# Performance work log

Hardware: AMD Instinct MI355X
Metric: run time of the kernel (lower is better)

## Reference

```python
import jax, jax.numpy as jnp
import numpy as np

B, T = 1024, 128
T_IN, A_IN, V_IN = 300, 74, 35
D = 128            # dim_capsule
H = D // 2
ROUTING = 3
LABEL = 1


def _glorot(key, shape):
    fan_out, fan_in = shape[-2], shape[-1]
    s = jnp.sqrt(2.0 / (fan_in + fan_out)).astype(jnp.float32)
    return jax.random.normal(key, shape, jnp.float32) * s


def setup_inputs() -> dict:
    k = iter(jax.random.split(jax.random.key(0), 40))
    inp = {}
    inp["text"] = jax.random.normal(next(k), (B, T, T_IN), jnp.float32)
    inp["audio"] = jax.random.normal(next(k), (B, T, A_IN), jnp.float32)
    inp["video"] = jax.random.normal(next(k), (B, T, V_IN), jnp.float32)
    # bidirectional encoder LSTMs (hidden = D//2 per direction); biases b = b_ih + b_hh
    for p, din in (("t", T_IN), ("a", A_IN), ("v", V_IN)):
        for d in ("f", "b"):
            inp[p + "_Wih_" + d] = _glorot(next(k), (4 * H, din))
            inp[p + "_Whh_" + d] = _glorot(next(k), (4 * H, H))
            inp[p + "_b_" + d] = jnp.zeros((4 * H,), jnp.float32)
    # 4 capsule projection matrices per modality, stacked [4, D, D]
    inp["Wt"] = _glorot(next(k), (4, D, D))
    inp["Wa"] = _glorot(next(k), (4, D, D))
    inp["Wv"] = _glorot(next(k), (4, D, D))
    # routing LSTMs (ta, tv, av, tav) stacked on leading axis
    inp["r_Wih"] = _glorot(next(k), (4, 4 * D, D))
    inp["r_Whh"] = _glorot(next(k), (4, 4 * D, D))
    inp["r_b"] = jnp.zeros((4, 4 * D), jnp.float32)
    # decision bidirectional LSTM (hidden = D per direction)
    for d in ("f", "b"):
        inp["d_Wih_" + d] = _glorot(next(k), (4 * D, D))
        inp["d_Whh_" + d] = _glorot(next(k), (4 * D, D))
        inp["d_b_" + d] = jnp.zeros((4 * D,), jnp.float32)
    inp["fc1_W"] = _glorot(next(k), (H, D))
    inp["fc1_b"] = jnp.zeros((H,), jnp.float32)
    inp["fc2_W"] = _glorot(next(k), (LABEL, H))
    inp["fc2_b"] = jnp.zeros((LABEL,), jnp.float32)
    inp["batch_size"] = B
    return inp


def _lstm_final(x, Wih, Whh, b):
    # x: [B, T, I] -> final hidden state [B, Hh]; torch gate order i, f, g, o
    Hh = Whh.shape[-1]
    z = jnp.zeros((x.shape[0], Hh), x.dtype)

    def step(carry, xt):
        h, c = carry
        g = xt @ Wih.T + h @ Whh.T + b
        i, f, gg, o = jnp.split(g, 4, axis=-1)
        c = jax.nn.sigmoid(f) * c + jax.nn.sigmoid(i) * jnp.tanh(gg)
        h = jax.nn.sigmoid(o) * jnp.tanh(c)
        return (h, c), None

    (h, _), _ = jax.lax.scan(step, (z, z), jnp.swapaxes(x, 0, 1))
    return h


def _forward(text, audio, video,
             t_Wih_f, t_Whh_f, t_b_f, t_Wih_b, t_Whh_b, t_b_b,
             a_Wih_f, a_Whh_f, a_b_f, a_Wih_b, a_Whh_b, a_b_b,
             v_Wih_f, v_Whh_f, v_b_f, v_Wih_b, v_Whh_b, v_b_b,
             Wt, Wa, Wv, r_Wih, r_Whh, r_b,
             d_Wih_f, d_Whh_f, d_b_f, d_Wih_b, d_Whh_b, d_b_b,
             fc1_W, fc1_b, fc2_W, fc2_b):
    Bsz = text.shape[0]

    def ctx(x, Wf, Uf, bf, Wb, Ub, bb):
        # biLSTM final hidden, fwd||bwd concat -> [B, 1, D]
        hf = _lstm_final(x, Wf, Uf, bf)
        hb = _lstm_final(x[:, ::-1], Wb, Ub, bb)
        return jnp.concatenate([hf, hb], -1)[:, None, :]

    tc = ctx(text, t_Wih_f, t_Whh_f, t_b_f, t_Wih_b, t_Whh_b, t_b_b)
    ac = ctx(audio, a_Wih_f, a_Whh_f, a_b_f, a_Wih_b, a_Whh_b, a_b_b)
    vc = ctx(video, v_Wih_f, v_Whh_f, v_b_f, v_Wih_b, v_Whh_b, v_b_b)

    tusc = jnp.einsum('bod,kde->kboe', tc, Wt)   # [4, B, 1, D]
    ausc = jnp.einsum('bod,kde->kboe', ac, Wa)
    vusc = jnp.einsum('bod,kde->kboe', vc, Wv)

    pre = [jnp.concatenate([tusc[0], ausc[0]], 1),                # ta  [B,2,D]
           jnp.concatenate([tusc[1], vusc[0]], 1),                # tv  [B,2,D]
           jnp.concatenate([ausc[1], vusc[1]], 1),                # av  [B,2,D]
           jnp.concatenate([tusc[2], ausc[2], vusc[2]], 1)]       # tav [B,3,D]

    rc = [jnp.ones((Bsz, n, D), text.dtype) for n in (2, 2, 2, 3, 7)]
    dc = None
    for r in range(ROUTING + 1):
        rc = [jax.nn.softmax(c, axis=1) for c in rc]
        # per-pair routing LSTMs, final hidden [B,1,D]
        bc = [_lstm_final(rc[i] * pre[i], r_Wih[i], r_Whh[i], r_b[i])[:, None, :]
              for i in range(4)]
        deci = jnp.concatenate([tusc[3], ausc[3], vusc[3]] + bc, 1)  # [B,7,D]
        xd = rc[4] * deci
        # decision biLSTM: sum of both directions' final hidden -> [B,1,D]
        dc = (_lstm_final(xd, d_Wih_f, d_Whh_f, d_b_f)
              + _lstm_final(xd[:, ::-1], d_Wih_b, d_Whh_b, d_b_b))[:, None, :]
        if r < ROUTING:
            # agreement update: bmm gives [B,n,1], broadcasts over last dim (== repeat)
            rc = [rc[i] + jnp.matmul(pre[i], jnp.swapaxes(bc[i], 1, 2)) for i in range(4)] \
                 + [rc[4] + jnp.matmul(deci, jnp.swapaxes(dc, 1, 2))]

    dc = dc[:, 0, :]
    o1 = jnp.tanh(dc @ fc1_W.T + fc1_b)
    return o1 @ fc2_W.T + fc2_b   # mosi: no output tanh


def reference(text, audio, video,
              t_Wih_f, t_Whh_f, t_b_f, t_Wih_b, t_Whh_b, t_b_b,
              a_Wih_f, a_Whh_f, a_b_f, a_Wih_b, a_Whh_b, a_b_b,
              v_Wih_f, v_Whh_f, v_b_f, v_Wih_b, v_Whh_b, v_b_b,
              Wt, Wa, Wv, r_Wih, r_Whh, r_b,
              d_Wih_f, d_Whh_f, d_b_f, d_Wih_b, d_Whh_b, d_b_b,
              fc1_W, fc1_b, fc2_W, fc2_b, batch_size):
    return _forward(text, audio, video,
                    t_Wih_f, t_Whh_f, t_b_f, t_Wih_b, t_Whh_b, t_b_b,
                    a_Wih_f, a_Whh_f, a_b_f, a_Wih_b, a_Whh_b, a_b_b,
                    v_Wih_f, v_Whh_f, v_b_f, v_Wih_b, v_Whh_b, v_b_b,
                    Wt, Wa, Wv, r_Wih, r_Whh, r_b,
                    d_Wih_f, d_Whh_f, d_b_f, d_Wih_b, d_Whh_b, d_b_b,
                    fc1_W, fc1_b, fc2_W, fc2_b)
```

## Files before the change

### kernel.cpp

```cpp
#include <hip/hip_runtime.h>

typedef __bf16 bf16;
typedef _Float16 f16;
typedef f16 f16x8 __attribute__((ext_vector_type(8)));
typedef float f32x4 __attribute__((ext_vector_type(4)));

__device__ __forceinline__ f32x4 mfma16h(f16x8 a, f16x8 b, f32x4 c) {
  return __builtin_amdgcn_mfma_f32_16x16x32_f16(a, b, c, 0, 0, 0);
}
__device__ __forceinline__ float sigm(float x) { return 1.0f / (1.0f + __expf(-x)); }
__device__ __forceinline__ float tanh_f(float x) {
  float e = __expf(-2.0f * fabsf(x));
  return copysignf((1.0f - e) / (1.0f + e), x);
}
__device__ __forceinline__ float ldin(const void* p, long i, int f32m) {
  if (f32m) return ((const float*)p)[i];
  unsigned u = (unsigned)((const unsigned short*)p)[i] << 16;
  return __uint_as_float(u);
}
__device__ __forceinline__ unsigned short f16u(f16 h) { return __builtin_bit_cast(unsigned short, h); }
__device__ __forceinline__ float bfc(unsigned short s) { return __uint_as_float((unsigned)s << 16); }

__global__ void detect_dtype(const unsigned short* __restrict__ p, int* __restrict__ flag) {
  __shared__ int cnt;
  if (threadIdx.x == 0) cnt = 0;
  __syncthreads();
  int c = 0;
  for (int i = threadIdx.x; i < 4096; i += 256) {
    unsigned e = (p[2 * i] >> 7) & 0xFFu;
    if (e >= 0xC0u) ++c;
  }
  atomicAdd(&cnt, c);
  __syncthreads();
  if (threadIdx.x == 0) *flag = (cnt > 64) ? 1 : 0;
}


struct PadArgs { const void* src[6]; };
__global__ void conv_pad(PadArgs a, f16* __restrict__ wo, const int* __restrict__ flag) {
  const int dinT[6] = {300, 300, 74, 74, 35, 35};
  const int kpT[6] = {320, 320, 96, 96, 64, 64};
  const int offT[6] = {0, 81920, 163840, 188416, 212992, 229376};
  int id = blockIdx.y;
  int din = dinT[id], kp = kpT[id];
  const void* s = a.src[id];
  f16* o = wo + offT[id];
  int f32m = *flag;
  int total = 256 * kp;
  for (int i = blockIdx.x * blockDim.x + threadIdx.x; i < total; i += gridDim.x * blockDim.x) {
    int n = i / kp, k = i - n * kp;
    float v = (k < din) ? ldin(s, n * din + k, f32m) : 0.0f;
    o[i] = (f16)v;
  }
}

struct HiloArgs { const void* src[12]; int n[12]; int off[12]; };
__global__ void conv_h16(HiloArgs a, f16* __restrict__ wo, const int* __restrict__ flag) {
  int j = blockIdx.y;
  int n = a.n[j];
  const void* s = a.src[j];
  f16* o = wo + a.off[j];
  int f32m = *flag;
  for (int i = blockIdx.x * blockDim.x + threadIdx.x; i < n; i += gridDim.x * blockDim.x)
    o[i] = (f16)ldin(s, i, f32m);
}

struct F32Args { const void* src[16]; int n[16]; int off[16]; };
__global__ void conv_f32(F32Args a, float* __restrict__ dst, const int* __restrict__ flag) {
  int j = blockIdx.y;
  int n = a.n[j];
  const void* s = a.src[j];
  float* d = dst + a.off[j];
  int f32m = *flag;
  for (int i = blockIdx.x * blockDim.x + threadIdx.x; i < n; i += gridDim.x * blockDim.x)
    d[i] = ldin(s, i, f32m);
}

__global__ void init_rc(float* __restrict__ rcs) {
  int i = blockIdx.x * 256 + threadIdx.x;
  if (i < 16384) rcs[i] = 1.0f;
}

struct TriArgs {
  const void* x[3];
  const f16* wAll;
  const float* fmisc;
  float* ctx;
  const int* flag;
};

template <int DIN, int KP, int CHUNK, int F32M>
__device__ void tri_body(const void* __restrict__ xsrc,
                         const f16* __restrict__ wp, const f16* __restrict__ whh,
                         const float* __restrict__ bias, float* __restrict__ ctx,
                         int m, int d, int b0, char* sm) {
  constexpr int XP = KP + 8;
  constexpr int NKS = KP / 32;
  constexpr int NCH = DIN / CHUNK;
  constexpr int ITER = (NCH + 15) / 16;

  f16 (*Xhi)[XP] = (f16 (*)[XP])sm;
  f16 (*Xlo)[XP] = (f16 (*)[XP])(sm + 32 * XP * 2);
  f16 (*hbuf)[16][72] = (f16 (*)[16][72])(sm + 64 * XP * 2);
  float* gbuf = (float*)(sm + 64 * XP * 2 + 4608);

  const int tid = threadIdx.x;
  const int lane = tid & 63, n16 = lane & 15, q = lane >> 4, w8 = tid >> 6;
  const int srow = tid & 31, sct = tid >> 5;
  const int hc = tid & 63, rr = tid >> 6;

  f16x8 wihr[2][NKS];
  f16x8 whr[2][2];
#pragma unroll
  for (int t = 0; t < 2; ++t) {
    int cc = (w8 + t * 8) * 16 + n16;
#pragma unroll
    for (int ks = 0; ks < NKS; ++ks)
      wihr[t][ks] = *(const f16x8*)(wp + cc * KP + ks * 32 + q * 8);
#pragma unroll
    for (int ks = 0; ks < 2; ++ks)
      whr[t][ks] = *(const f16x8*)(whh + cc * 64 + ks * 32 + q * 8);
  }
  float bgm[4];
#pragma unroll
  for (int g = 0; g < 4; ++g) bgm[g] = bias[g * 64 + hc];

  {
    unsigned* z = (unsigned*)sm;
    int nz = (64 * XP * 2 + 4608) >> 2;
    for (int i = tid; i < nz; i += 512) z[i] = 0u;
  }

  uint4 pf[ITER];
  auto stage_load = [&](int tg) {
#pragma unroll
    for (int i = 0; i < ITER; ++i) {
      int c = sct + i * 16;
      if (c < NCH) {
        int tl = srow >> 4, bb = srow & 15;
        int t = tg * 2 + tl; if (d) t = 127 - t;
        long base = ((long)(b0 + bb) * 128 + t) * DIN + c * CHUNK;
        if (F32M) {
          const float* p = (const float*)xsrc + base;
          if constexpr (CHUNK == 4) pf[i] = *(const uint4*)p;
          else if constexpr (CHUNK == 2) { uint2 v = *(const uint2*)p; pf[i].x = v.x; pf[i].y = v.y; }
          else pf[i].x = *(const unsigned*)p;
        } else {
          const unsigned short* p = (const unsigned short*)xsrc + base;
          if constexpr (CHUNK == 4) { uint2 v = *(const uint2*)p; pf[i].x = v.x; pf[i].y = v.y; }
          else if constexpr (CHUNK == 2) pf[i].x = *(const unsigned*)p;
          else pf[i].x = *p;
        }
      }
    }
  };
  auto stage_store = [&]() {
#pragma unroll
    for (int i = 0; i < ITER; ++i) {
      int c = sct + i * 16;
      if (c < NCH) {
        float v[4];
        if (F32M) {
          v[0] = __uint_as_float(pf[i].x); v[1] = __uint_as_float(pf[i].y);
// ... 84 lines not shown
      float c = sigm(gf) * c2[e] + sigm(gi) * tanh_f(gg);
      c2[e] = c;
      float h = sigm(go) * tanh_f(c);
      hbuf[1][row][hc] = (f16)h;
    }
    __syncthreads();

    {
      f16x8 h0 = *(const f16x8*)(&hbuf[1][n16][q * 8]);
      f16x8 h1 = *(const f16x8*)(&hbuf[1][n16][32 + q * 8]);
      a10 = mfma16h(h0, whr[0][0], a10); a10 = mfma16h(h1, whr[0][1], a10);
      a11 = mfma16h(h0, whr[1][0], a11); a11 = mfma16h(h1, whr[1][1], a11);
    }
#pragma unroll
    for (int e = 0; e < 4; ++e) {
      gbuf[(q * 4 + e) * 260 + w8 * 16 + n16] = a10[e];
      gbuf[(q * 4 + e) * 260 + 128 + w8 * 16 + n16] = a11[e];
    }
    __syncthreads();

    const bool lastStep = (tg == 63);
#pragma unroll
    for (int e = 0; e < 2; ++e) {
      int row = rr + e * 8;
      float gi = gbuf[row * 260 + hc] + bgm[0];
      float gf = gbuf[row * 260 + 64 + hc] + bgm[1];
      float gg = gbuf[row * 260 + 128 + hc] + bgm[2];
      float go = gbuf[row * 260 + 192 + hc] + bgm[3];
      float c = sigm(gf) * c2[e] + sigm(gi) * tanh_f(gg);
      c2[e] = c;
      float h = sigm(go) * tanh_f(c);
      hbuf[0][row][hc] = (f16)h;
      if (lastStep) ctx[(m * 1024 + b0 + row) * 128 + d * 64 + hc] = h;
    }
  }
}

__global__ __launch_bounds__(512, 2) void tri_lstm(TriArgs A) {
  __shared__ __align__(16) char sm[64 * 328 * 2 + 4608 + 16640];
  int bid = blockIdx.x;
  int md = bid >> 6, xb = bid & 63;
  int m = md >> 1, d = md & 1, b0 = xb * 16;
  const int wpOffT[6] = {0, 81920, 163840, 188416, 212992, 229376};
  const f16* wp = A.wAll + wpOffT[md];
  const f16* whh = A.wAll + 245760 + md * 16384;
  const float* bias = A.fmisc + md * 256;
  int f32m = *A.flag;
  if (f32m) {
    if (m == 0)      tri_body<300, 320, 4, 1>(A.x[0], wp, whh, bias, A.ctx, m, d, b0, sm);
    else if (m == 1) tri_body<74, 96, 2, 1>(A.x[1], wp, whh, bias, A.ctx, m, d, b0, sm);
    else             tri_body<35, 64, 1, 1>(A.x[2], wp, whh, bias, A.ctx, m, d, b0, sm);
  } else {
    if (m == 0)      tri_body<300, 320, 4, 0>(A.x[0], wp, whh, bias, A.ctx, m, d, b0, sm);
    else if (m == 1) tri_body<74, 96, 2, 0>(A.x[1], wp, whh, bias, A.ctx, m, d, b0, sm);
    else             tri_body<35, 64, 1, 0>(A.x[2], wp, whh, bias, A.ctx, m, d, b0, sm);
  }
}

__global__ __launch_bounds__(128) void usc_kern(const float* __restrict__ ctx,
                                                const float* __restrict__ fmisc,
                                                float* __restrict__ usc) {
  __shared__ float cr[4][128];
  int b0 = blockIdx.x * 4;
  int mk = blockIdx.y, mod = mk >> 2;
  int e = threadIdx.x;
  const float* W = fmisc + 4608 + mk * 16384;
  for (int i = e; i < 512; i += 128) {
    int r = i >> 7, dd = i & 127;
    cr[r][dd] = ctx[(mod * 1024 + b0 + r) * 128 + dd];
  }
  __syncthreads();
  float a0 = 0.f, a1 = 0.f, a2 = 0.f, a3 = 0.f;
  for (int dd = 0; dd < 128; ++dd) {
    float wv = W[dd * 128 + e];
    a0 += cr[0][dd] * wv; a1 += cr[1][dd] * wv;
    a2 += cr[2][dd] * wv; a3 += cr[3][dd] * wv;
  }
  usc[(mk * 1024 + b0 + 0) * 128 + e] = a0;
  usc[(mk * 1024 + b0 + 1) * 128 + e] = a1;
  usc[(mk * 1024 + b0 + 2) * 128 + e] = a2;
  usc[(mk * 1024 + b0 + 3) * 128 + e] = a3;
}

#define LSTM_STEP_DECL \
  const int tid = threadIdx.x; \
  const int lane = tid & 63, n16 = lane & 15, q = lane >> 4, w = tid >> 6; \
  const int u = w * 16 + n16; \
  const int u2 = tid & 127, rgg = tid >> 7;

__device__ __forceinline__ void lstm_step_mfma(
    f32x4* acc, const f16 (*xh)[16][136], const f16 (*xl)[16][136],
    const f16 (*hh)[16][136], int p,
    const f16* __restrict__ Wih, const f16x8 (*whf)[4],
    int n16, int q, int u) {
#pragma unroll
  for (int ks = 0; ks < 4; ++ks) {
    f16x8 axh = *(const f16x8*)(&xh[p][n16][ks * 32 + q * 8]);
    f16x8 axl = *(const f16x8*)(&xl[p][n16][ks * 32 + q * 8]);
    f16x8 ahh = *(const f16x8*)(&hh[p][n16][ks * 32 + q * 8]);
#pragma unroll
    for (int g = 0; g < 4; ++g) {
      f16x8 bh = *(const f16x8*)(Wih + (g * 128 + u) * 128 + ks * 32 + q * 8);
      acc[g] = mfma16h(axh, bh, acc[g]);
      acc[g] = mfma16h(axl, bh, acc[g]);
      acc[g] = mfma16h(ahh, whf[g][ks], acc[g]);
    }
  }
}

__global__ __launch_bounds__(512) void rchain(const float* __restrict__ usc,
                                              const float* __restrict__ rcs,
                                              const f16* __restrict__ wAll,
                                              const float* __restrict__ fmisc,
                                              float* __restrict__ bcg) {
  __shared__ __align__(16) f16 xh[2][16][136], xl[2][16][136], hh[2][16][136];
  __shared__ float rcl[16][3];
  LSTM_STEP_DECL
  const int chain = blockIdx.y;
  const int b0 = blockIdx.x * 16;
  const int WihOff[4] = {344064, 409600, 475136, 540672};
  const int WhhOff[4] = {606208, 671744, 737280, 802816};
  const int bOff[4] = {1536, 2048, 2560, 3072};
  const int ns = (chain == 3) ? 3 : 2;

  if (tid < 16) {
    int row = tid;
    int goff = (chain == 3) ? 6 : chain * 2;
    float v[3], mx = -1e30f;
    for (int j = 0; j < ns; ++j) { v[j] = rcs[(b0 + row) * 16 + goff + j]; mx = fmaxf(mx, v[j]); }
    float s = 0.f;
    for (int j = 0; j < ns; ++j) { v[j] = __expf(v[j] - mx); s += v[j]; }
    float inv = 1.0f / s;
    for (int j = 0; j < ns; ++j) rcl[row][j] = v[j] * inv;
  }
  for (int i = tid; i < 2 * 16 * 136; i += 512) (&hh[0][0][0])[i] = (f16)0.0f;

  const f16* Whh = wAll + WhhOff[chain];
  f16x8 whf[4][4];
#pragma unroll
  for (int g = 0; g < 4; ++g)
#pragma unroll
    for (int ks = 0; ks < 4; ++ks)
      whf[g][ks] = *(const f16x8*)(Whh + (g * 128 + u) * 128 + ks * 32 + q * 8);
  const f16* Wih = wAll + WihOff[chain];
  const float* bias = fmisc + bOff[chain];
  float bg[4];
#pragma unroll
  for (int g = 0; g < 4; ++g) bg[g] = bias[g * 128 + u];

  const int preMk0[4] = {0, 1, 5, 2};
  const int preMk1[4] = {4, 8, 9, 6};
  float creg[4] = {0.f, 0.f, 0.f, 0.f};
  __syncthreads();

  for (int s = 0; s < ns; ++s) {
    int p = s & 1;
    int mk = (s == 0) ? preMk0[chain] : (s == 1 ? preMk1[chain] : 10);
#pragma unroll
    for (int rr = 0; rr < 4; ++rr) {
      int row = rgg * 4 + rr;
      float pv = usc[(mk * 1024 + b0 + row) * 128 + u2];
      float xv = rcl[row][s] * pv;
      f16 xhv = (f16)xv;
      xh[p][row][u2] = xhv;
      xl[p][row][u2] = (f16)(xv - (float)xhv);
    }
    __syncthreads();
    f32x4 acc[4];
    const f32x4 zf = {0.f, 0.f, 0.f, 0.f};
#pragma unroll
    for (int g = 0; g < 4; ++g) acc[g] = zf;
    lstm_step_mfma(acc, xh, xl, hh, p, Wih, whf, n16, q, u);
#pragma unroll
    for (int e = 0; e < 4; ++e) {
      int row = q * 4 + e;
      float gi = acc[0][e] + bg[0];
      float gf = acc[1][e] + bg[1];
      float gg = acc[2][e] + bg[2];
      float go = acc[3][e] + bg[3];
      float c = sigm(gf) * creg[e] + sigm(gi) * tanh_f(gg);
      creg[e] = c;
      float h = sigm(go) * tanh_f(c);
      hh[p ^ 1][row][u] = (f16)h;
      if (s == ns - 1) bcg[(chain * 1024 + b0 + row) * 128 + u] = h;
    }
  }
}

__global__ __launch_bounds__(512) void decision(const float* __restrict__ usc,
                                                const float* __restrict__ rcs,
                                                const f16* __restrict__ wAll,
                                                const float* __restrict__ fmisc,
                                                const float* __restrict__ bcg,
                                                float* __restrict__ dcF,
                                                float* __restrict__ dcB) {
  __shared__ __align__(16) f16 xh[2][16][136], xl[2][16][136], hh[2][16][136];
  __shared__ float rcl[16][7];
  LSTM_STEP_DECL
  const int dir = blockIdx.y;
  const int b0 = blockIdx.x * 16;

  if (tid < 16) {
    int row = tid;
    float v[7], mx = -1e30f;
    for (int j = 0; j < 7; ++j) { v[j] = rcs[(b0 + row) * 16 + 9 + j]; mx = fmaxf(mx, v[j]); }
    float s = 0.f;
    for (int j = 0; j < 7; ++j) { v[j] = __expf(v[j] - mx); s += v[j]; }
    float inv = 1.0f / s;
    for (int j = 0; j < 7; ++j) rcl[row][j] = v[j] * inv;
  }
  for (int i = tid; i < 2 * 16 * 136; i += 512) (&hh[0][0][0])[i] = (f16)0.0f;

  const int WihOffD[2] = {868352, 999424};
  const int WhhOffD[2] = {933888, 1064960};
  const int bOffD[2] = {3584, 4096};
  const f16* Whh = wAll + WhhOffD[dir];
  f16x8 whf[4][4];
#pragma unroll
  for (int g = 0; g < 4; ++g)
#pragma unroll
    for (int ks = 0; ks < 4; ++ks)
      whf[g][ks] = *(const f16x8*)(Whh + (g * 128 + u) * 128 + ks * 32 + q * 8);
  const f16* Wih = wAll + WihOffD[dir];
  const float* bias = fmisc + bOffD[dir];
  float bg[4];
#pragma unroll
  for (int g = 0; g < 4; ++g) bg[g] = bias[g * 128 + u];

  const int dmk[3] = {3, 7, 11};
  float creg[4] = {0.f, 0.f, 0.f, 0.f};
  __syncthreads();

  for (int s = 0; s < 7; ++s) {
    int p = s & 1;
    int j = dir ? (6 - s) : s;
#pragma unroll
    for (int rr = 0; rr < 4; ++rr) {
      int row = rgg * 4 + rr;
      float pv = (j < 3) ? usc[(dmk[j] * 1024 + b0 + row) * 128 + u2]
                         : bcg[((j - 3) * 1024 + b0 + row) * 128 + u2];
      float xv = rcl[row][j] * pv;
      f16 xhv = (f16)xv;
      xh[p][row][u2] = xhv;
      xl[p][row][u2] = (f16)(xv - (float)xhv);
    }
    __syncthreads();
    f32x4 acc[4];
    const f32x4 zf = {0.f, 0.f, 0.f, 0.f};
#pragma unroll
    for (int g = 0; g < 4; ++g) acc[g] = zf;
    lstm_step_mfma(acc, xh, xl, hh, p, Wih, whf, n16, q, u);
#pragma unroll
    for (int e = 0; e < 4; ++e) {
      int row = q * 4 + e;
      float gi = acc[0][e] + bg[0];
      float gf = acc[1][e] + bg[1];
      float gg = acc[2][e] + bg[2];
      float go = acc[3][e] + bg[3];
      float c = sigm(gf) * creg[e] + sigm(gi) * tanh_f(gg);
      creg[e] = c;
      float h = sigm(go) * tanh_f(c);
      hh[p ^ 1][row][u] = (f16)h;
      if (s == 6) {
        if (dir == 0) dcF[(b0 + row) * 128 + u] = h;
        else dcB[(b0 + row) * 128 + u] = h;
      }
    }
  }
}

__global__ __launch_bounds__(256) void rupdate(const float* __restrict__ usc,
                                               const float* __restrict__ bcg,
                                               const float* __restrict__ dcF,
                                               const float* __restrict__ dcB,
                                               float* __restrict__ rcs,
                                               float* __restrict__ dcw, int last) {
  __shared__ float dsum[16][128];
  __shared__ float rcl[16][16];
  const int tid = threadIdx.x;
  const int b0 = blockIdx.x * 16;
  for (int i = tid; i < 2048; i += 256) {
    int row = i >> 7, col = i & 127;
    float v = dcF[(b0 + row) * 128 + col] + dcB[(b0 + row) * 128 + col];
    dsum[row][col] = v;
    if (last) dcw[(b0 + row) * 128 + col] = v;
  }
  {
    int row = tid >> 4, cap = tid & 15;
    rcl[row][cap] = rcs[(b0 + row) * 16 + cap];
  }
  __syncthreads();
  if (!last) {
    int row = tid >> 4, cap = tid & 15;
    const int goffT[16] = {0, 0, 2, 2, 4, 4, 6, 6, 6, 9, 9, 9, 9, 9, 9, 9};
    const int gnT[16] = {2, 2, 2, 2, 2, 2, 3, 3, 3, 7, 7, 7, 7, 7, 7, 7};
    int go = goffT[cap], gn = gnT[cap];
    float mx = -1e30f;
    for (int j = 0; j < gn; ++j) mx = fmaxf(mx, rcl[row][go + j]);
    float s = 0.f;
    for (int j = 0; j < gn; ++j) s += __expf(rcl[row][go + j] - mx);
    float sm = __expf(rcl[row][cap] - mx) / s;

    const int preMkTab[9] = {0, 4, 1, 8, 5, 9, 2, 6, 10};
    float a = 0.f;
    if (cap < 9) {
      int i = (cap < 6) ? (cap >> 1) : 3;
      const float* pr = usc + (preMkTab[cap] * 1024 + b0 + row) * 128;
      const float* bcrow = bcg + (i * 1024 + b0 + row) * 128;
      for (int dd = 0; dd < 128; ++dd) a += pr[dd] * bcrow[dd];
    } else {
      int j = cap - 9;
      if (j < 3) {
        const int dmk[3] = {3, 7, 11};
        const float* pr = usc + (dmk[j] * 1024 + b0 + row) * 128;
        for (int dd = 0; dd < 128; ++dd) a += pr[dd] * dsum[row][dd];
      } else {
        const float* bcrow = bcg + ((j - 3) * 1024 + b0 + row) * 128;
        for (int dd = 0; dd < 128; ++dd) a += bcrow[dd] * dsum[row][dd];
      }
    }
    rcs[(b0 + row) * 16 + cap] = sm + a;
  }
}

__global__ __launch_bounds__(64) void head(const float* __restrict__ dc, const float* __restrict__ fcw,
                                           void* __restrict__ out, const int* __restrict__ flag) {
  int b = blockIdx.x, j = threadIdx.x;
  const float* r = dc + b * 128;
  float acc = fcw[209408 + j];
  for (int dd = 0; dd < 128; ++dd) acc += r[dd] * fcw[201216 + j * 128 + dd];
  float o = tanh_f(acc) * fcw[209472 + j];
  for (int off = 32; off; off >>= 1) o += __shfl_down(o, off, 64);
  if (j == 0) {
    float res = o + fcw[209536];
    if (*flag) ((float*)out)[b] = res;
    else ((bf16*)out)[b] = (bf16)res;
  }
}

extern "C" void kernel_launch(void* const* d_in, const int* in_sizes, int n_in,
                              void* d_out, int out_size, void* d_ws, size_t ws_size,
                              hipStream_t stream) {
  float* fw = (float*)d_ws;
  int* flag = (int*)d_ws;
  float* ctx = fw + 4;
  float* usc = ctx + 393216;
  float* dcw = usc + 1572864;
  float* fmisc = dcw + 131072;
  float* rcs = fmisc + 209552;
  float* bcg = rcs + 16384;
  float* dcF = bcg + 524288;
  float* dcB = dcF + 131072;
  f16* wAll = (f16*)(dcB + 131072);

  hipLaunchKernelGGL(detect_dtype, dim3(1), dim3(256), 0, stream,
                     (const unsigned short*)d_in[0], flag);

  PadArgs pa;
  HiloArgs ha;
  for (int m = 0; m < 3; ++m)
    for (int dd = 0; dd < 2; ++dd) {
      int md = m * 6 + dd * 3;
      pa.src[m * 2 + dd] = d_in[3 + md + 0];
      ha.src[m * 2 + dd] = d_in[3 + md + 1];
      ha.n[m * 2 + dd] = 16384;
      ha.off[m * 2 + dd] = 245760 + (m * 2 + dd) * 16384;
    }
  const int hsrc[6] = {24, 25, 27, 28, 30, 31};
  const int hn[6] = {262144, 262144, 65536, 65536, 65536, 65536};
  const int hoff[6] = {344064, 606208, 868352, 933888, 999424, 1064960};
  for (int j = 0; j < 6; ++j) { ha.src[6 + j] = d_in[hsrc[j]]; ha.n[6 + j] = hn[j]; ha.off[6 + j] = hoff[j]; }
  hipLaunchKernelGGL(conv_pad, dim3(64, 6), dim3(256), 0, stream, pa, wAll, (const int*)flag);
  hipLaunchKernelGGL(conv_h16, dim3(128, 12), dim3(256), 0, stream, ha, wAll, (const int*)flag);

  F32Args fa;
  for (int m = 0; m < 3; ++m)
    for (int dd = 0; dd < 2; ++dd) {
      fa.src[m * 2 + dd] = d_in[3 + m * 6 + dd * 3 + 2];
      fa.n[m * 2 + dd] = 256;
      fa.off[m * 2 + dd] = (m * 2 + dd) * 256;
    }
  const int fsrc[10] = {26, 29, 32, 21, 22, 23, 33, 34, 35, 36};
  const int fn[10] = {2048, 512, 512, 65536, 65536, 65536, 8192, 64, 64, 1};
  const int foff[10] = {1536, 3584, 4096, 4608, 70144, 135680, 201216, 209408, 209472, 209536};
  for (int j = 0; j < 10; ++j) { fa.src[6 + j] = d_in[fsrc[j]]; fa.n[6 + j] = fn[j]; fa.off[6 + j] = foff[j]; }
  hipLaunchKernelGGL(conv_f32, dim3(64, 16), dim3(256), 0, stream, fa, fmisc, (const int*)flag);
  hipLaunchKernelGGL(init_rc, dim3(64), dim3(256), 0, stream, rcs);

  TriArgs ta;
  ta.x[0] = d_in[0]; ta.x[1] = d_in[1]; ta.x[2] = d_in[2];
  ta.wAll = wAll; ta.fmisc = fmisc; ta.ctx = ctx; ta.flag = flag;
  hipLaunchKernelGGL(tri_lstm, dim3(384), dim3(512), 0, stream, ta);

  hipLaunchKernelGGL(usc_kern, dim3(256, 12), dim3(128), 0, stream,
                     (const float*)ctx, (const float*)fmisc, usc);

  for (int r = 0; r < 4; ++r) {
    hipLaunchKernelGGL(rchain, dim3(64, 4), dim3(512), 0, stream,
                       (const float*)usc, (const float*)rcs, (const f16*)wAll,
                       (const float*)fmisc, bcg);
    hipLaunchKernelGGL(decision, dim3(64, 2), dim3(512), 0, stream,
                       (const float*)usc, (const float*)rcs, (const f16*)wAll,
                       (const float*)fmisc, (const float*)bcg, dcF, dcB);
    hipLaunchKernelGGL(rupdate, dim3(64), dim3(256), 0, stream,
                       (const float*)usc, (const float*)bcg, (const float*)dcF,
                       (const float*)dcB, rcs, dcw, (r == 3) ? 1 : 0);
  }

  hipLaunchKernelGGL(head, dim3(1024), dim3(64), 0, stream,
                     (const float*)dcw, (const float*)fmisc, d_out, (const int*)flag);
}
```

Measured before the change: 848.2 us.

## Fuse routing iterations into one persistent per-batch-tile kernel

```diff
diff --git a/kernel.cpp b/kernel.cpp
--- a/kernel.cpp
+++ b/kernel.cpp
@@ -74,11 +74,6 @@
   int f32m = *flag;
   for (int i = blockIdx.x * blockDim.x + threadIdx.x; i < n; i += gridDim.x * blockDim.x)
     d[i] = ldin(s, i, f32m);
-}
-
-__global__ void init_rc(float* __restrict__ rcs) {
-  int i = blockIdx.x * 256 + threadIdx.x;
-  if (i < 16384) rcs[i] = 1.0f;
 }
 
 struct TriArgs {
@@ -329,12 +324,6 @@
   usc[(mk * 1024 + b0 + 3) * 128 + e] = a3;
 }
 
-#define LSTM_STEP_DECL \
-  const int tid = threadIdx.x; \
-  const int lane = tid & 63, n16 = lane & 15, q = lane >> 4, w = tid >> 6; \
-  const int u = w * 16 + n16; \
-  const int u2 = tid & 127, rgg = tid >> 7;
-
 __device__ __forceinline__ void lstm_step_mfma(
     f32x4* acc, const f16 (*xh)[16][136], const f16 (*xl)[16][136],
     const f16 (*hh)[16][136], int p,
@@ -355,218 +344,208 @@
   }
 }
 
-__global__ __launch_bounds__(512) void rchain(const float* __restrict__ usc,
-                                              const float* __restrict__ rcs,
-                                              const f16* __restrict__ wAll,
-                                              const float* __restrict__ fmisc,
-                                              float* __restrict__ bcg) {
+__global__ __launch_bounds__(512) void routing(const float* __restrict__ usc,
+                                               const f16* __restrict__ wAll,
+                                               const float* __restrict__ fmisc,
+                                               float* __restrict__ bcg,
+                                               float* __restrict__ dcw) {
   __shared__ __align__(16) f16 xh[2][16][136], xl[2][16][136], hh[2][16][136];
-  __shared__ float rcl[16][3];
-  LSTM_STEP_DECL
-  const int chain = blockIdx.y;
+  __shared__ float rcsS[16][16];
+  __shared__ float rclC[16][7];
+  __shared__ float dcFs[16][128], dcBs[16][128];
+  const int tid = threadIdx.x;
+  const int lane = tid & 63, n16 = lane & 15, q = lane >> 4, w = tid >> 6;
+  const int u = w * 16 + n16;
+  const int u2 = tid & 127, rgg = tid >> 7;
   const int b0 = blockIdx.x * 16;
+
   const int WihOff[4] = {344064, 409600, 475136, 540672};
   const int WhhOff[4] = {606208, 671744, 737280, 802816};
   const int bOff[4] = {1536, 2048, 2560, 3072};
-  const int ns = (chain == 3) ? 3 : 2;
-
-  if (tid < 16) {
-    int row = tid;
-    int goff = (chain == 3) ? 6 : chain * 2;
-    float v[3], mx = -1e30f;
-    for (int j = 0; j < ns; ++j) { v[j] = rcs[(b0 + row) * 16 + goff + j]; mx = fmaxf(mx, v[j]); }
-    float s = 0.f;
-    for (int j = 0; j < ns; ++j) { v[j] = __expf(v[j] - mx); s += v[j]; }
-    float inv = 1.0f / s;
-    for (int j = 0; j < ns; ++j) rcl[row][j] = v[j] * inv;
-  }
-  for (int i = tid; i < 2 * 16 * 136; i += 512) (&hh[0][0][0])[i] = (f16)0.0f;
-
-  const f16* Whh = wAll + WhhOff[chain];
-  f16x8 whf[4][4];
-#pragma unroll
-  for (int g = 0; g < 4; ++g)
-#pragma unroll
-    for (int ks = 0; ks < 4; ++ks)
-      whf[g][ks] = *(const f16x8*)(Whh + (g * 128 + u) * 128 + ks * 32 + q * 8);
-  const f16* Wih = wAll + WihOff[chain];
-  const float* bias = fmisc + bOff[chain];
-  float bg[4];
-#pragma unroll
-  for (int g = 0; g < 4; ++g) bg[g] = bias[g * 128 + u];
-
   const int preMk0[4] = {0, 1, 5, 2};
   const int preMk1[4] = {4, 8, 9, 6};
-  float creg[4] = {0.f, 0.f, 0.f, 0.f};
-  __syncthreads();
-
-  for (int s = 0; s < ns; ++s) {
-    int p = s & 1;
-    int mk = (s == 0) ? preMk0[chain] : (s == 1 ? preMk1[chain] : 10);
-#pragma unroll
-    for (int rr = 0; rr < 4; ++rr) {
-      int row = rgg * 4 + rr;
-      float pv = usc[(mk * 1024 + b0 + row) * 128 + u2];
-      float xv = rcl[row][s] * pv;
-      f16 xhv = (f16)xv;
-      xh[p][row][u2] = xhv;
-      xl[p][row][u2] = (f16)(xv - (float)xhv);
-    }
-    __syncthreads();
-    f32x4 acc[4];
-    const f32x4 zf = {0.f, 0.f, 0.f, 0.f};
-#pragma unroll
-    for (int g = 0; g < 4; ++g) acc[g] = zf;
-    lstm_step_mfma(acc, xh, xl, hh, p, Wih, whf, n16, q, u);
-#pragma unroll
-    for (int e = 0; e < 4; ++e) {
-      int row = q * 4 + e;
-      float gi = acc[0][e] + bg[0];
-      float gf = acc[1][e] + bg[1];
-      float gg = acc[2][e] + bg[2];
-      float go = acc[3][e] + bg[3];
-      float c = sigm(gf) * creg[e] + sigm(gi) * tanh_f(gg);
-      creg[e] = c;
-      float h = sigm(go) * tanh_f(c);
-      hh[p ^ 1][row][u] = (f16)h;
-      if (s == ns - 1) bcg[(chain * 1024 + b0 + row) * 128 + u] = h;
-    }
-  }
-}
-
-__global__ __launch_bounds__(512) void decision(const float* __restrict__ usc,
-                                                const float* __restrict__ rcs,
-                                                const f16* __restrict__ wAll,
-                                                const float* __restrict__ fmisc,
-                                                const float* __restrict__ bcg,
-                                                float* __restrict__ dcF,
-                                                float* __restrict__ dcB) {
-  __shared__ __align__(16) f16 xh[2][16][136], xl[2][16][136], hh[2][16][136];
-  __shared__ float rcl[16][7];
-  LSTM_STEP_DECL
-  const int dir = blockIdx.y;
-  const int b0 = blockIdx.x * 16;
-
-  if (tid < 16) {
-    int row = tid;
-    float v[7], mx = -1e30f;
-    for (int j = 0; j < 7; ++j) { v[j] = rcs[(b0 + row) * 16 + 9 + j]; mx = fmaxf(mx, v[j]); }
-    float s = 0.f;
-    for (int j = 0; j < 7; ++j) { v[j] = __expf(v[j] - mx); s += v[j]; }
-    float inv = 1.0f / s;
-    for (int j = 0; j < 7; ++j) rcl[row][j] = v[j] * inv;
-  }
-  for (int i = tid; i < 2 * 16 * 136; i += 512) (&hh[0][0][0])[i] = (f16)0.0f;
-
+  const int dmk[3] = {3, 7, 11};
   const int WihOffD[2] = {868352, 999424};
   const int WhhOffD[2] = {933888, 1064960};
   const int bOffD[2] = {3584, 4096};
-  const f16* Whh = wAll + WhhOffD[dir];
-  f16x8 whf[4][4];
-#pragma unroll
-  for (int g = 0; g < 4; ++g)
-#pragma unroll
-    for (int ks = 0; ks < 4; ++ks)
-      whf[g][ks] = *(const f16x8*)(Whh + (g * 128 + u) * 128 + ks * 32 + q * 8);
-  const f16* Wih = wAll + WihOffD[dir];
-  const float* bias = fmisc + bOffD[dir];
-  float bg[4];
-#pragma unroll
-  for (int g = 0; g < 4; ++g) bg[g] = bias[g * 128 + u];
-
-  const int dmk[3] = {3, 7, 11};
-  float creg[4] = {0.f, 0.f, 0.f, 0.f};
-  __syncthreads();
-
-  for (int s = 0; s < 7; ++s) {
-    int p = s & 1;
-    int j = dir ? (6 - s) : s;
-#pragma unroll
-    for (int rr = 0; rr < 4; ++rr) {
-      int row = rgg * 4 + rr;
-      float pv = (j < 3) ? usc[(dmk[j] * 1024 + b0 + row) * 128 + u2]
-                         : bcg[((j - 3) * 1024 + b0 + row) * 128 + u2];
-      float xv = rcl[row][j] * pv;
-      f16 xhv = (f16)xv;
-      xh[p][row][u2] = xhv;
-      xl[p][row][u2] = (f16)(xv - (float)xhv);
-    }
-    __syncthreads();
-    f32x4 acc[4];
-    const f32x4 zf = {0.f, 0.f, 0.f, 0.f};
-#pragma unroll
-    for (int g = 0; g < 4; ++g) acc[g] = zf;
-    lstm_step_mfma(acc, xh, xl, hh, p, Wih, whf, n16, q, u);
-#pragma unroll
-    for (int e = 0; e < 4; ++e) {
-      int row = q * 4 + e;
-      float gi = acc[0][e] + bg[0];
-      float gf = acc[1][e] + bg[1];
-      float gg = acc[2][e] + bg[2];
-      float go = acc[3][e] + bg[3];
-      float c = sigm(gf) * creg[e] + sigm(gi) * tanh_f(gg);
-      creg[e] = c;
-      float h = sigm(go) * tanh_f(c);
-      hh[p ^ 1][row][u] = (f16)h;
-      if (s == 6) {
-        if (dir == 0) dcF[(b0 + row) * 128 + u] = h;
-        else dcB[(b0 + row) * 128 + u] = h;
-      }
-    }
-  }
-}
-
-__global__ __launch_bounds__(256) void rupdate(const float* __restrict__ usc,
-                                               const float* __restrict__ bcg,
-                                               const float* __restrict__ dcF,
-                                               const float* __restrict__ dcB,
-                                               float* __restrict__ rcs,
-                                               float* __restrict__ dcw, int last) {
-  __shared__ float dsum[16][128];
-  __shared__ float rcl[16][16];
-  const int tid = threadIdx.x;
-  const int b0 = blockIdx.x * 16;
-  for (int i = tid; i < 2048; i += 256) {
-    int row = i >> 7, col = i & 127;
-    float v = dcF[(b0 + row) * 128 + col] + dcB[(b0 + row) * 128 + col];
-    dsum[row][col] = v;
-    if (last) dcw[(b0 + row) * 128 + col] = v;
-  }
-  {
-    int row = tid >> 4, cap = tid & 15;
-    rcl[row][cap] = rcs[(b0 + row) * 16 + cap];
-  }
-  __syncthreads();
-  if (!last) {
-    int row = tid >> 4, cap = tid & 15;
-    const int goffT[16] = {0, 0, 2, 2, 4, 4, 6, 6, 6, 9, 9, 9, 9, 9, 9, 9};
-    const int gnT[16] = {2, 2, 2, 2, 2, 2, 3, 3, 3, 7, 7, 7, 7, 7, 7, 7};
-    int go = goffT[cap], gn = gnT[cap];
-    float mx = -1e30f;
-    for (int j = 0; j < gn; ++j) mx = fmaxf(mx, rcl[row][go + j]);
-    float s = 0.f;
-    for (int j = 0; j < gn; ++j) s += __expf(rcl[row][go + j] - mx);
-    float sm = __expf(rcl[row][cap] - mx) / s;
-
-    const int preMkTab[9] = {0, 4, 1, 8, 5, 9, 2, 6, 10};
-    float a = 0.f;
-    if (cap < 9) {
-      int i = (cap < 6) ? (cap >> 1) : 3;
-      const float* pr = usc + (preMkTab[cap] * 1024 + b0 + row) * 128;
-      const float* bcrow = bcg + (i * 1024 + b0 + row) * 128;
-      for (int dd = 0; dd < 128; ++dd) a += pr[dd] * bcrow[dd];
+
+  if (tid < 256) rcsS[tid >> 4][tid & 15] = 1.0f;
+
+  for (int r = 0; r < 4; ++r) {
+    for (int chain = 0; chain < 4; ++chain) {
+      const int ns = (chain == 3) ? 3 : 2;
+      __syncthreads();
+      if (tid < 16) {
+        int row = tid;
+        int goff = (chain == 3) ? 6 : chain * 2;
+        float v[3], mx = -1e30f;
+        for (int j = 0; j < ns; ++j) { v[j] = rcsS[row][goff + j]; mx = fmaxf(mx, v[j]); }
+        float s = 0.f;
+        for (int j = 0; j < ns; ++j) { v[j] = __expf(v[j] - mx); s += v[j]; }
+        float inv = 1.0f / s;
+        for (int j = 0; j < ns; ++j) rclC[row][j] = v[j] * inv;
+      }
+      for (int i = tid; i < 2 * 16 * 136; i += 512) (&hh[0][0][0])[i] = (f16)0.0f;
+
+      const f16* Whh = wAll + WhhOff[chain];
+      f16x8 whf[4][4];
+#pragma unroll
+      for (int g = 0; g < 4; ++g)
+#pragma unroll
+        for (int ks = 0; ks < 4; ++ks)
+          whf[g][ks] = *(const f16x8*)(Whh + (g * 128 + u) * 128 + ks * 32 + q * 8);
+      const f16* Wih = wAll + WihOff[chain];
+      const float* bias = fmisc + bOff[chain];
+      float bg[4];
+#pragma unroll
+      for (int g = 0; g < 4; ++g) bg[g] = bias[g * 128 + u];
+
+      float creg[4] = {0.f, 0.f, 0.f, 0.f};
+      __syncthreads();
+
+      for (int s = 0; s < ns; ++s) {
+        int p = s & 1;
+        int mk = (s == 0) ? preMk0[chain] : (s == 1 ? preMk1[chain] : 10);
+#pragma unroll
+        for (int rr = 0; rr < 4; ++rr) {
+          int row = rgg * 4 + rr;
+          float pv = usc[(mk * 1024 + b0 + row) * 128 + u2];
+          float xv = rclC[row][s] * pv;
+          f16 xhv = (f16)xv;
+          xh[p][row][u2] = xhv;
+          xl[p][row][u2] = (f16)(xv - (float)xhv);
+        }
+        __syncthreads();
+        f32x4 acc[4];
+        const f32x4 zf = {0.f, 0.f, 0.f, 0.f};
+#pragma unroll
+        for (int g = 0; g < 4; ++g) acc[g] = zf;
+        lstm_step_mfma(acc, xh, xl, hh, p, Wih, whf, n16, q, u);
+#pragma unroll
+        for (int e = 0; e < 4; ++e) {
+          int row = q * 4 + e;
+          float gi = acc[0][e] + bg[0];
+          float gf = acc[1][e] + bg[1];
+          float gg = acc[2][e] + bg[2];
+          float go = acc[3][e] + bg[3];
+          float c = sigm(gf) * creg[e] + sigm(gi) * tanh_f(gg);
+          creg[e] = c;
+          float h = sigm(go) * tanh_f(c);
+          hh[p ^ 1][row][u] = (f16)h;
+          if (s == ns - 1) bcg[(chain * 1024 + b0 + row) * 128 + u] = h;
+        }
+      }
+      __syncthreads();
+    }
+
+    for (int dir = 0; dir < 2; ++dir) {
+      __syncthreads();
+      if (tid < 16) {
+        int row = tid;
+        float v[7], mx = -1e30f;
+        for (int j = 0; j < 7; ++j) { v[j] = rcsS[row][9 + j]; mx = fmaxf(mx, v[j]); }
+        float s = 0.f;
+        for (int j = 0; j < 7; ++j) { v[j] = __expf(v[j] - mx); s += v[j]; }
+        float inv = 1.0f / s;
+        for (int j = 0; j < 7; ++j) rclC[row][j] = v[j] * inv;
+      }
+      for (int i = tid; i < 2 * 16 * 136; i += 512) (&hh[0][0][0])[i] = (f16)0.0f;
+
+      const f16* Whh = wAll + WhhOffD[dir];
+      f16x8 whf[4][4];
+#pragma unroll
+      for (int g = 0; g < 4; ++g)
+#pragma unroll
+        for (int ks = 0; ks < 4; ++ks)
+          whf[g][ks] = *(const f16x8*)(Whh + (g * 128 + u) * 128 + ks * 32 + q * 8);
+      const f16* Wih = wAll + WihOffD[dir];
+      const float* bias = fmisc + bOffD[dir];
+      float bg[4];
+#pragma unroll
+      for (int g = 0; g < 4; ++g) bg[g] = bias[g * 128 + u];
+
+      float creg[4] = {0.f, 0.f, 0.f, 0.f};
+      __syncthreads();
+
+      for (int s = 0; s < 7; ++s) {
+        int p = s & 1;
+        int j = dir ? (6 - s) : s;
+#pragma unroll
+        for (int rr = 0; rr < 4; ++rr) {
+          int row = rgg * 4 + rr;
+          float pv = (j < 3) ? usc[(dmk[j] * 1024 + b0 + row) * 128 + u2]
+                             : bcg[((j - 3) * 1024 + b0 + row) * 128 + u2];
+          float xv = rclC[row][j] * pv;
+          f16 xhv = (f16)xv;
+          xh[p][row][u2] = xhv;
+          xl[p][row][u2] = (f16)(xv - (float)xhv);
+        }
+        __syncthreads();
+        f32x4 acc[4];
+        const f32x4 zf = {0.f, 0.f, 0.f, 0.f};
+#pragma unroll
+        for (int g = 0; g < 4; ++g) acc[g] = zf;
+        lstm_step_mfma(acc, xh, xl, hh, p, Wih, whf, n16, q, u);
+#pragma unroll
+        for (int e = 0; e < 4; ++e) {
+          int row = q * 4 + e;
+          float gi = acc[0][e] + bg[0];
+          float gf = acc[1][e] + bg[1];
+          float gg = acc[2][e] + bg[2];
+          float go = acc[3][e] + bg[3];
+          float c = sigm(gf) * creg[e] + sigm(gi) * tanh_f(gg);
+          creg[e] = c;
+          float h = sigm(go) * tanh_f(c);
+          hh[p ^ 1][row][u] = (f16)h;
+          if (s == 6) {
+            if (dir == 0) dcFs[row][u] = h;
+            else dcBs[row][u] = h;
+          }
+        }
+      }
+      __syncthreads();
+    }
+
+    if (r == 3) {
+      for (int i = tid; i < 2048; i += 512) {
+        int row = i >> 7, col = i & 127;
+        dcw[(b0 + row) * 128 + col] = dcFs[row][col] + dcBs[row][col];
+      }
     } else {
-      int j = cap - 9;
-      if (j < 3) {
-        const int dmk[3] = {3, 7, 11};
-        const float* pr = usc + (dmk[j] * 1024 + b0 + row) * 128;
-        for (int dd = 0; dd < 128; ++dd) a += pr[dd] * dsum[row][dd];
-      } else {
-        const float* bcrow = bcg + ((j - 3) * 1024 + b0 + row) * 128;
-        for (int dd = 0; dd < 128; ++dd) a += bcrow[dd] * dsum[row][dd];
-      }
-    }
-    rcs[(b0 + row) * 16 + cap] = sm + a;
+      float newv = 0.f;
+      int row = tid >> 4, cap = tid & 15;
+      if (tid < 256) {
+        const int goffT[16] = {0, 0, 2, 2, 4, 4, 6, 6, 6, 9, 9, 9, 9, 9, 9, 9};
+        const int gnT[16] = {2, 2, 2, 2, 2, 2, 3, 3, 3, 7, 7, 7, 7, 7, 7, 7};
+        int go = goffT[cap], gn = gnT[cap];
+        float mx = -1e30f;
+        for (int j = 0; j < gn; ++j) mx = fmaxf(mx, rcsS[row][go + j]);
+        float s = 0.f;
+        for (int j = 0; j < gn; ++j) s += __expf(rcsS[row][go + j] - mx);
+        float sm = __expf(rcsS[row][cap] - mx) / s;
+
+        const int preMkTab[9] = {0, 4, 1, 8, 5, 9, 2, 6, 10};
+        float a = 0.f;
+        if (cap < 9) {
+          int i = (cap < 6) ? (cap >> 1) : 3;
+          const float* pr = usc + (preMkTab[cap] * 1024 + b0 + row) * 128;
+          const float* bcrow = bcg + (i * 1024 + b0 + row) * 128;
+          for (int dd = 0; dd < 128; ++dd) a += pr[dd] * bcrow[dd];
+        } else {
+          int j = cap - 9;
+          if (j < 3) {
+            const float* pr = usc + (dmk[j] * 1024 + b0 + row) * 128;
+            for (int dd = 0; dd < 128; ++dd) a += pr[dd] * (dcFs[row][dd] + dcBs[row][dd]);
+          } else {
+            const float* bcrow = bcg + ((j - 3) * 1024 + b0 + row) * 128;
+            for (int dd = 0; dd < 128; ++dd) a += bcrow[dd] * (dcFs[row][dd] + dcBs[row][dd]);
+          }
+        }
+        newv = sm + a;
+      }
+      __syncthreads();
+      if (tid < 256) rcsS[row][cap] = newv;
+    }
   }
 }
 
@@ -632,7 +611,6 @@
   const int foff[10] = {1536, 3584, 4096, 4608, 70144, 135680, 201216, 209408, 209472, 209536};
   for (int j = 0; j < 10; ++j) { fa.src[6 + j] = d_in[fsrc[j]]; fa.n[6 + j] = fn[j]; fa.off[6 + j] = foff[j]; }
   hipLaunchKernelGGL(conv_f32, dim3(64, 16), dim3(256), 0, stream, fa, fmisc, (const int*)flag);
-  hipLaunchKernelGGL(init_rc, dim3(64), dim3(256), 0, stream, rcs);
 
   TriArgs ta;
   ta.x[0] = d_in[0]; ta.x[1] = d_in[1]; ta.x[2] = d_in[2];
@@ -642,17 +620,9 @@
   hipLaunchKernelGGL(usc_kern, dim3(256, 12), dim3(128), 0, stream,
                      (const float*)ctx, (const float*)fmisc, usc);
 
-  for (int r = 0; r < 4; ++r) {
-    hipLaunchKernelGGL(rchain, dim3(64, 4), dim3(512), 0, stream,
-                       (const float*)usc, (const float*)rcs, (const f16*)wAll,
-                       (const float*)fmisc, bcg);
-    hipLaunchKernelGGL(decision, dim3(64, 2), dim3(512), 0, stream,
-                       (const float*)usc, (const float*)rcs, (const f16*)wAll,
-                       (const float*)fmisc, (const float*)bcg, dcF, dcB);
-    hipLaunchKernelGGL(rupdate, dim3(64), dim3(256), 0, stream,
-                       (const float*)usc, (const float*)bcg, (const float*)dcF,
-                       (const float*)dcB, rcs, dcw, (r == 3) ? 1 : 0);
-  }
+  hipLaunchKernelGGL(routing, dim3(64), dim3(512), 0, stream,
+                     (const float*)usc, (const f16*)wAll, (const float*)fmisc,
+                     bcg, dcw);
 
   hipLaunchKernelGGL(head, dim3(1024), dim3(64), 0, stream,
                      (const float*)dcw, (const float*)fmisc, d_out, (const int*)flag);
```

New measurement: 1.085 ms. +27.9%, slower.

## Merge conversion kernels, keep input weights in registers, prefetch next-step inputs

Applied to the files above, without the earlier changes.

```diff
diff --git a/kernel.cpp b/kernel.cpp
--- a/kernel.cpp
+++ b/kernel.cpp
@@ -37,43 +37,42 @@
 
 
 struct PadArgs { const void* src[6]; };
-__global__ void conv_pad(PadArgs a, f16* __restrict__ wo, const int* __restrict__ flag) {
-  const int dinT[6] = {300, 300, 74, 74, 35, 35};
-  const int kpT[6] = {320, 320, 96, 96, 64, 64};
-  const int offT[6] = {0, 81920, 163840, 188416, 212992, 229376};
-  int id = blockIdx.y;
-  int din = dinT[id], kp = kpT[id];
-  const void* s = a.src[id];
-  f16* o = wo + offT[id];
-  int f32m = *flag;
-  int total = 256 * kp;
-  for (int i = blockIdx.x * blockDim.x + threadIdx.x; i < total; i += gridDim.x * blockDim.x) {
-    int n = i / kp, k = i - n * kp;
-    float v = (k < din) ? ldin(s, n * din + k, f32m) : 0.0f;
-    o[i] = (f16)v;
-  }
-}
-
 struct HiloArgs { const void* src[12]; int n[12]; int off[12]; };
-__global__ void conv_h16(HiloArgs a, f16* __restrict__ wo, const int* __restrict__ flag) {
-  int j = blockIdx.y;
-  int n = a.n[j];
-  const void* s = a.src[j];
-  f16* o = wo + a.off[j];
-  int f32m = *flag;
-  for (int i = blockIdx.x * blockDim.x + threadIdx.x; i < n; i += gridDim.x * blockDim.x)
-    o[i] = (f16)ldin(s, i, f32m);
-}
-
 struct F32Args { const void* src[16]; int n[16]; int off[16]; };
-__global__ void conv_f32(F32Args a, float* __restrict__ dst, const int* __restrict__ flag) {
-  int j = blockIdx.y;
-  int n = a.n[j];
-  const void* s = a.src[j];
-  float* d = dst + a.off[j];
-  int f32m = *flag;
-  for (int i = blockIdx.x * blockDim.x + threadIdx.x; i < n; i += gridDim.x * blockDim.x)
-    d[i] = ldin(s, i, f32m);
+
+__global__ void conv_all(PadArgs pa, HiloArgs ha, F32Args fa,
+                         f16* __restrict__ wo, float* __restrict__ fm,
+                         const int* __restrict__ flag) {
+  const int y = blockIdx.y;
+  const int f32m = *flag;
+  if (y < 6) {
+    const int dinT[6] = {300, 300, 74, 74, 35, 35};
+    const int kpT[6] = {320, 320, 96, 96, 64, 64};
+    const int offT[6] = {0, 81920, 163840, 188416, 212992, 229376};
+    int din = dinT[y], kp = kpT[y];
+    const void* s = pa.src[y];
+    f16* o = wo + offT[y];
+    int total = 256 * kp;
+    for (int i = blockIdx.x * blockDim.x + threadIdx.x; i < total; i += gridDim.x * blockDim.x) {
+      int n = i / kp, k = i - n * kp;
+      float v = (k < din) ? ldin(s, n * din + k, f32m) : 0.0f;
+      o[i] = (f16)v;
+    }
+  } else if (y < 18) {
+    int j = y - 6;
+    int n = ha.n[j];
+    const void* s = ha.src[j];
+    f16* o = wo + ha.off[j];
+    for (int i = blockIdx.x * blockDim.x + threadIdx.x; i < n; i += gridDim.x * blockDim.x)
+      o[i] = (f16)ldin(s, i, f32m);
+  } else {
+    int j = y - 18;
+    int n = fa.n[j];
+    const void* s = fa.src[j];
+    float* d = fm + fa.off[j];
+    for (int i = blockIdx.x * blockDim.x + threadIdx.x; i < n; i += gridDim.x * blockDim.x)
+      d[i] = ldin(s, i, f32m);
+  }
 }
 
 __global__ void init_rc(float* __restrict__ rcs) {
@@ -335,11 +334,11 @@
   const int u = w * 16 + n16; \
   const int u2 = tid & 127, rgg = tid >> 7;
 
-__device__ __forceinline__ void lstm_step_mfma(
+__device__ __forceinline__ void lstm_step_mfma_r(
     f32x4* acc, const f16 (*xh)[16][136], const f16 (*xl)[16][136],
     const f16 (*hh)[16][136], int p,
-    const f16* __restrict__ Wih, const f16x8 (*whf)[4],
-    int n16, int q, int u) {
+    const f16x8 (*bhf)[4], const f16x8 (*whf)[4],
+    int n16, int q) {
 #pragma unroll
   for (int ks = 0; ks < 4; ++ks) {
     f16x8 axh = *(const f16x8*)(&xh[p][n16][ks * 32 + q * 8]);
@@ -347,9 +346,8 @@
     f16x8 ahh = *(const f16x8*)(&hh[p][n16][ks * 32 + q * 8]);
 #pragma unroll
     for (int g = 0; g < 4; ++g) {
-      f16x8 bh = *(const f16x8*)(Wih + (g * 128 + u) * 128 + ks * 32 + q * 8);
-      acc[g] = mfma16h(axh, bh, acc[g]);
-      acc[g] = mfma16h(axl, bh, acc[g]);
+      acc[g] = mfma16h(axh, bhf[g][ks], acc[g]);
+      acc[g] = mfma16h(axl, bhf[g][ks], acc[g]);
       acc[g] = mfma16h(ahh, whf[g][ks], acc[g]);
     }
   }
@@ -383,13 +381,15 @@
   for (int i = tid; i < 2 * 16 * 136; i += 512) (&hh[0][0][0])[i] = (f16)0.0f;
 
   const f16* Whh = wAll + WhhOff[chain];
-  f16x8 whf[4][4];
+  const f16* Wih = wAll + WihOff[chain];
+  f16x8 whf[4][4], bhf[4][4];
 #pragma unroll
   for (int g = 0; g < 4; ++g)
 #pragma unroll
-    for (int ks = 0; ks < 4; ++ks)
+    for (int ks = 0; ks < 4; ++ks) {
       whf[g][ks] = *(const f16x8*)(Whh + (g * 128 + u) * 128 + ks * 32 + q * 8);
-  const f16* Wih = wAll + WihOff[chain];
+      bhf[g][ks] = *(const f16x8*)(Wih + (g * 128 + u) * 128 + ks * 32 + q * 8);
+    }
   const float* bias = fmisc + bOff[chain];
   float bg[4];
 #pragma unroll
@@ -398,26 +398,38 @@
   const int preMk0[4] = {0, 1, 5, 2};
   const int preMk1[4] = {4, 8, 9, 6};
   float creg[4] = {0.f, 0.f, 0.f, 0.f};
+
+  float pv[4];
+  {
+    int mk0 = preMk0[chain];
+#pragma unroll
+    for (int rr = 0; rr < 4; ++rr)
+      pv[rr] = usc[(mk0 * 1024 + b0 + rgg * 4 + rr) * 128 + u2];
+  }
   __syncthreads();
 
   for (int s = 0; s < ns; ++s) {
     int p = s & 1;
-    int mk = (s == 0) ? preMk0[chain] : (s == 1 ? preMk1[chain] : 10);
 #pragma unroll
     for (int rr = 0; rr < 4; ++rr) {
       int row = rgg * 4 + rr;
-      float pv = usc[(mk * 1024 + b0 + row) * 128 + u2];
-      float xv = rcl[row][s] * pv;
+      float xv = rcl[row][s] * pv[rr];
       f16 xhv = (f16)xv;
       xh[p][row][u2] = xhv;
       xl[p][row][u2] = (f16)(xv - (float)xhv);
     }
+    if (s + 1 < ns) {
+      int mk2 = (s + 1 == 1) ? preMk1[chain] : 10;
+#pragma unroll
+      for (int rr = 0; rr < 4; ++rr)
+        pv[rr] = usc[(mk2 * 1024 + b0 + rgg * 4 + rr) * 128 + u2];
+    }
     __syncthreads();
     f32x4 acc[4];
     const f32x4 zf = {0.f, 0.f, 0.f, 0.f};
 #pragma unroll
     for (int g = 0; g < 4; ++g) acc[g] = zf;
-    lstm_step_mfma(acc, xh, xl, hh, p, Wih, whf, n16, q, u);
+    lstm_step_mfma_r(acc, xh, xl, hh, p, bhf, whf, n16, q);
 #pragma unroll
     for (int e = 0; e < 4; ++e) {
       int row = q * 4 + e;
@@ -462,13 +474,15 @@
   const int WhhOffD[2] = {933888, 1064960};
   const int bOffD[2] = {3584, 4096};
   const f16* Whh = wAll + WhhOffD[dir];
-  f16x8 whf[4][4];
+  const f16* Wih = wAll + WihOffD[dir];
+  f16x8 whf[4][4], bhf[4][4];
 #pragma unroll
   for (int g = 0; g < 4; ++g)
 #pragma unroll
-    for (int ks = 0; ks < 4; ++ks)
+    for (int ks = 0; ks < 4; ++ks) {
       whf[g][ks] = *(const f16x8*)(Whh + (g * 128 + u) * 128 + ks * 32 + q * 8);
-  const f16* Wih = wAll + WihOffD[dir];
+      bhf[g][ks] = *(const f16x8*)(Wih + (g * 128 + u) * 128 + ks * 32 + q * 8);
+    }
   const float* bias = fmisc + bOffD[dir];
   float bg[4];
 #pragma unroll
@@ -476,6 +490,17 @@
 
   const int dmk[3] = {3, 7, 11};
   float creg[4] = {0.f, 0.f, 0.f, 0.f};
+
+  float pv[4];
+  {
+    int j0 = dir ? 6 : 0;
+#pragma unroll
+    for (int rr = 0; rr < 4; ++rr) {
+      int row = rgg * 4 + rr;
+      pv[rr] = (j0 < 3) ? usc[(dmk[j0] * 1024 + b0 + row) * 128 + u2]
+                        : bcg[((j0 - 3) * 1024 + b0 + row) * 128 + u2];
+    }
+  }
   __syncthreads();
 
   for (int s = 0; s < 7; ++s) {
@@ -484,19 +509,26 @@
 #pragma unroll
     for (int rr = 0; rr < 4; ++rr) {
       int row = rgg * 4 + rr;
-      float pv = (j < 3) ? usc[(dmk[j] * 1024 + b0 + row) * 128 + u2]
-                         : bcg[((j - 3) * 1024 + b0 + row) * 128 + u2];
-      float xv = rcl[row][j] * pv;
+      float xv = rcl[row][j] * pv[rr];
       f16 xhv = (f16)xv;
       xh[p][row][u2] = xhv;
       xl[p][row][u2] = (f16)(xv - (float)xhv);
     }
+    if (s < 6) {
+      int j2 = dir ? (5 - s) : (s + 1);
+#pragma unroll
+      for (int rr = 0; rr < 4; ++rr) {
+        int row = rgg * 4 + rr;
+        pv[rr] = (j2 < 3) ? usc[(dmk[j2] * 1024 + b0 + row) * 128 + u2]
+                          : bcg[((j2 - 3) * 1024 + b0 + row) * 128 + u2];
+      }
+    }
     __syncthreads();
     f32x4 acc[4];
     const f32x4 zf = {0.f, 0.f, 0.f, 0.f};
 #pragma unroll
     for (int g = 0; g < 4; ++g) acc[g] = zf;
-    lstm_step_mfma(acc, xh, xl, hh, p, Wih, whf, n16, q, u);
+    lstm_step_mfma_r(acc, xh, xl, hh, p, bhf, whf, n16, q);
 #pragma unroll
     for (int e = 0; e < 4; ++e) {
       int row = q * 4 + e;
@@ -617,8 +649,6 @@
   const int hn[6] = {262144, 262144, 65536, 65536, 65536, 65536};
   const int hoff[6] = {344064, 606208, 868352, 933888, 999424, 1064960};
   for (int j = 0; j < 6; ++j) { ha.src[6 + j] = d_in[hsrc[j]]; ha.n[6 + j] = hn[j]; ha.off[6 + j] = hoff[j]; }
-  hipLaunchKernelGGL(conv_pad, dim3(64, 6), dim3(256), 0, stream, pa, wAll, (const int*)flag);
-  hipLaunchKernelGGL(conv_h16, dim3(128, 12), dim3(256), 0, stream, ha, wAll, (const int*)flag);
 
   F32Args fa;
   for (int m = 0; m < 3; ++m)
@@ -631,7 +661,9 @@
   const int fn[10] = {2048, 512, 512, 65536, 65536, 65536, 8192, 64, 64, 1};
   const int foff[10] = {1536, 3584, 4096, 4608, 70144, 135680, 201216, 209408, 209472, 209536};
   for (int j = 0; j < 10; ++j) { fa.src[6 + j] = d_in[fsrc[j]]; fa.n[6 + j] = fn[j]; fa.off[6 + j] = foff[j]; }
-  hipLaunchKernelGGL(conv_f32, dim3(64, 16), dim3(256), 0, stream, fa, fmisc, (const int*)flag);
+
+  hipLaunchKernelGGL(conv_all, dim3(64, 34), dim3(256), 0, stream,
+                     pa, ha, fa, wAll, fmisc, (const int*)flag);
   hipLaunchKernelGGL(init_rc, dim3(64), dim3(256), 0, stream, rcs);
 
   TriArgs ta;
```

New measurement: 803.6 us. -5.3%, faster.
